# Kernel tuning notes

Measured on AMD Instinct MI355X. Metric: run time of the kernel, lower is better.

Reference implementation:

```python
import jax, jax.numpy as jnp
import numpy as np

N_NODES = 100000
N_EDGES = 600000
FEAT_DIM = 128


def setup_inputs() -> dict:
    key = jax.random.key(0)
    k_x, k_e, k_w1, k_b1, k_w2, k_b2 = jax.random.split(key, 6)
    x = jax.random.normal(k_x, (N_NODES, FEAT_DIM), dtype=jnp.float32)
    edge_index = jax.random.randint(k_e, (2, N_EDGES), 0, N_NODES, dtype=jnp.int64)
    # nn.Linear default init: U(-1/sqrt(fan_in), 1/sqrt(fan_in))
    lim1 = 1.0 / np.sqrt(2 * FEAT_DIM)
    lim2 = 1.0 / np.sqrt(FEAT_DIM)
    W1 = jax.random.uniform(k_w1, (2 * FEAT_DIM, FEAT_DIM), minval=-lim1, maxval=lim1, dtype=jnp.float32)
    b1 = jax.random.uniform(k_b1, (FEAT_DIM,), minval=-lim1, maxval=lim1, dtype=jnp.float32)
    W2 = jax.random.uniform(k_w2, (FEAT_DIM, 1), minval=-lim2, maxval=lim2, dtype=jnp.float32)
    b2 = jax.random.uniform(k_b2, (1,), minval=-lim2, maxval=lim2, dtype=jnp.float32)
    return {"x": x, "edge_index": edge_index, "W1": W1, "b1": b1, "W2": W2, "b2": b2}


def reference(x, edge_index, W1, b1, W2, b2):
    row, col = edge_index[0], edge_index[1]
    # gather endpoint features and concat -> [E, 2*feat_dim]
    edge_feat = jnp.concatenate([x[row], x[col]], axis=1)
    h = jax.nn.relu(edge_feat @ W1 + b1)  # [E, feat_dim]
    return jax.nn.sigmoid(h @ W2 + b2)    # [E, 1]
```

## Files before the change

kernel.cpp:

```cpp
#include <hip/hip_runtime.h>
#include <stdint.h>

#define N_NODES 100000
#define N_EDGES 600000
#define FEAT 128
#define BLK_M 128

typedef __attribute__((ext_vector_type(8))) short short8;
typedef __attribute__((ext_vector_type(4))) float floatx4;
typedef __attribute__((ext_vector_type(2))) float floatx2;

__device__ __forceinline__ short f2bf(float f) {
    unsigned u = __builtin_bit_cast(unsigned, f);
    u = (u + 0x7FFFu + ((u >> 16) & 1u)) >> 16;
    return (short)u;
}

__global__ __launch_bounds__(512, 4) void node_gemm_kernel(
    const float* __restrict__ x, const float* __restrict__ w1,
    const float* __restrict__ b1, unsigned char* __restrict__ y)
{
    __shared__ short lds_b[16 * 256 * 8];

    const int tid  = threadIdx.x;
    const int lane = tid & 63;
    const int wave = tid >> 6;
    const int nl   = lane & 15;
    const int q    = lane >> 4;
    const int m0   = blockIdx.x * BLK_M + wave * 16;

    const int node = m0 + nl;
    const int nsrc = (node < N_NODES) ? node : 0;
    floatx4 xv[8];
#pragma unroll
    for (int s = 0; s < 4; ++s) {
        const float* p = x + (size_t)nsrc * FEAT + s * 32 + q * 8;
        xv[2 * s]     = *(const floatx4*)(p);
        xv[2 * s + 1] = *(const floatx4*)(p + 4);
    }

#pragma unroll
    for (int it = 0; it < 8; ++it) {
        int t = it * 512 + tid;
        int n = t & 255, c = t >> 8;
        const float* src = (n < 128) ? (w1 + (c * 8) * 128 + n)
                                     : (w1 + (128 + c * 8) * 128 + (n - 128));
        short8 v;
#pragma unroll
        for (int j = 0; j < 8; ++j) v[j] = f2bf(src[j * 128]);
        *(short8*)(lds_b + t * 8) = v;
    }

    __syncthreads();

    short8 a[4];
#pragma unroll
    for (int s = 0; s < 4; ++s) {
        short8 av;
#pragma unroll
        for (int j = 0; j < 8; ++j) av[j] = f2bf(xv[2 * s + (j >> 2)][j & 3]);
        a[s] = av;
    }

    floatx4 acc[16];
#pragma unroll
    for (int nt = 0; nt < 16; ++nt) acc[nt] = (floatx4)(0.0f);

#pragma unroll
    for (int s = 0; s < 4; ++s) {
        const int crow = (s * 4 + q) << 8;
#pragma unroll
        for (int nt = 0; nt < 16; ++nt) {
            short8 wf = *(const short8*)(lds_b + ((crow + nt * 16 + nl) << 3));
            acc[nt] = __builtin_amdgcn_mfma_f32_16x16x32_bf16(wf, a[s], acc[nt], 0, 0, 0);
        }
    }

    if (node < N_NODES) {
        unsigned char* yr = y + (size_t)node * 256 + q * 4;
#pragma unroll
        for (int nt = 0; nt < 8; ++nt) {
            floatx4 bb = *(const floatx4*)(b1 + nt * 16 + q * 4);
            int d = __builtin_amdgcn_cvt_pk_fp8_f32(acc[nt][0] + bb[0],
                                                    acc[nt][1] + bb[1], 0, false);
            d = __builtin_amdgcn_cvt_pk_fp8_f32(acc[nt][2] + bb[2],
                                                acc[nt][3] + bb[3], d, true);
            *(int*)(yr + nt * 16) = d;
        }
#pragma unroll
        for (int nt = 8; nt < 16; ++nt) {
            int d = __builtin_amdgcn_cvt_pk_fp8_f32(acc[nt][0], acc[nt][1], 0, false);
            d = __builtin_amdgcn_cvt_pk_fp8_f32(acc[nt][2], acc[nt][3], d, true);
            *(int*)(yr + nt * 16) = d;
        }
    }
}

__device__ __forceinline__ void dec8(uint2 w, float* f) {
    floatx2 p0 = __builtin_amdgcn_cvt_pk_f32_fp8(w.x, false);
    floatx2 p1 = __builtin_amdgcn_cvt_pk_f32_fp8(w.x, true);
    floatx2 p2 = __builtin_amdgcn_cvt_pk_f32_fp8(w.y, false);
    floatx2 p3 = __builtin_amdgcn_cvt_pk_f32_fp8(w.y, true);
    f[0] = p0.x; f[1] = p0.y; f[2] = p1.x; f[3] = p1.y;
    f[4] = p2.x; f[5] = p2.y; f[6] = p3.x; f[7] = p3.y;
}

__global__ __launch_bounds__(256) void edge_kernel(
    const unsigned char* __restrict__ y, const int* __restrict__ eidx,
    const float* __restrict__ w2, const float* __restrict__ b2,
    float* __restrict__ out)
{
    const int l = threadIdx.x & 15;

    float w2r[8];
#pragma unroll
    for (int j = 0; j < 8; ++j) w2r[j] = w2[l * 8 + j];
    const float bias2 = b2[0];

    const int slot   = blockIdx.x * 16 + (threadIdx.x >> 4);
    const int nslots = gridDim.x * 16;

    for (int eb = slot * 4; eb < N_EDGES; eb += nslots * 4) {
        int4 rr = *(const int4*)(eidx + eb);
        int4 cc = *(const int4*)(eidx + N_EDGES + eb);

        uint2 u0 = *(const uint2*)(y + (size_t)rr.x * 256 + l * 8);
        uint2 u1 = *(const uint2*)(y + (size_t)rr.y * 256 + l * 8);
        uint2 u2 = *(const uint2*)(y + (size_t)rr.z * 256 + l * 8);
        uint2 u3 = *(const uint2*)(y + (size_t)rr.w * 256 + l * 8);
        uint2 v0 = *(const uint2*)(y + (size_t)cc.x * 256 + 128 + l * 8);
        uint2 v1 = *(const uint2*)(y + (size_t)cc.y * 256 + 128 + l * 8);
        uint2 v2 = *(const uint2*)(y + (size_t)cc.z * 256 + 128 + l * 8);
        uint2 v3 = *(const uint2*)(y + (size_t)cc.w * 256 + 128 + l * 8);

        float fu[8], fv[8];
        float p0 = 0.0f, p1 = 0.0f, p2 = 0.0f, p3 = 0.0f;

        dec8(u0, fu); dec8(v0, fv);
#pragma unroll
        for (int j = 0; j < 8; ++j)
            p0 = fmaf(fmaxf(fu[j] + fv[j], 0.0f), w2r[j], p0);
        dec8(u1, fu); dec8(v1, fv);
#pragma unroll
        for (int j = 0; j < 8; ++j)
            p1 = fmaf(fmaxf(fu[j] + fv[j], 0.0f), w2r[j], p1);
        dec8(u2, fu); dec8(v2, fv);
#pragma unroll
        for (int j = 0; j < 8; ++j)
            p2 = fmaf(fmaxf(fu[j] + fv[j], 0.0f), w2r[j], p2);
        dec8(u3, fu); dec8(v3, fv);
#pragma unroll
        for (int j = 0; j < 8; ++j)
            p3 = fmaf(fmaxf(fu[j] + fv[j], 0.0f), w2r[j], p3);

#pragma unroll
        for (int d = 1; d < 16; d <<= 1) {
            p0 += __shfl_xor(p0, d);
            p1 += __shfl_xor(p1, d);
            p2 += __shfl_xor(p2, d);
            p3 += __shfl_xor(p3, d);
        }

        if (l == 0) {
            floatx4 o;
            o[0] = 1.0f / (1.0f + __expf(-(p0 + bias2)));
            o[1] = 1.0f / (1.0f + __expf(-(p1 + bias2)));
            o[2] = 1.0f / (1.0f + __expf(-(p2 + bias2)));
            o[3] = 1.0f / (1.0f + __expf(-(p3 + bias2)));
            *(floatx4*)(out + eb) = o;
        }
    }
}

extern "C" void kernel_launch(void* const* d_in, const int* in_sizes, int n_in,
                              void* d_out, int out_size, void* d_ws, size_t ws_size,
                              hipStream_t stream) {
    const float* x  = (const float*)d_in[0];
    const int*   ei = (const int*)d_in[1];
    const float* W1 = (const float*)d_in[2];
    const float* b1 = (const float*)d_in[3];
    const float* W2 = (const float*)d_in[4];
    const float* b2 = (const float*)d_in[5];
    float* out = (float*)d_out;

    unsigned char* yq = (unsigned char*)d_ws;

    int mblocks = (N_NODES + BLK_M - 1) / BLK_M;
    node_gemm_kernel<<<mblocks, 512, 0, stream>>>(x, W1, b1, yq);

    edge_kernel<<<2048, 256, 0, stream>>>(yq, ei, W2, b2, out);
}
```

Before: 137.7 us.

## Make node GEMM persistent with register prefetch of next tile's x rows

```diff
diff --git a/kernel.cpp b/kernel.cpp
--- a/kernel.cpp
+++ b/kernel.cpp
@@ -5,6 +5,8 @@
 #define N_EDGES 600000
 #define FEAT 128
 #define BLK_M 128
+#define NT 782
+#define GRID_G 256
 
 typedef __attribute__((ext_vector_type(8))) short short8;
 typedef __attribute__((ext_vector_type(4))) float floatx4;
@@ -16,7 +18,7 @@
     return (short)u;
 }
 
-__global__ __launch_bounds__(512, 4) void node_gemm_kernel(
+__global__ __launch_bounds__(512, 2) void node_gemm_kernel(
     const float* __restrict__ x, const float* __restrict__ w1,
     const float* __restrict__ b1, unsigned char* __restrict__ y)
 {
@@ -27,17 +29,6 @@
     const int wave = tid >> 6;
     const int nl   = lane & 15;
     const int q    = lane >> 4;
-    const int m0   = blockIdx.x * BLK_M + wave * 16;
-
-    const int node = m0 + nl;
-    const int nsrc = (node < N_NODES) ? node : 0;
-    floatx4 xv[8];
-#pragma unroll
-    for (int s = 0; s < 4; ++s) {
-        const float* p = x + (size_t)nsrc * FEAT + s * 32 + q * 8;
-        xv[2 * s]     = *(const floatx4*)(p);
-        xv[2 * s + 1] = *(const floatx4*)(p + 4);
-    }
 
 #pragma unroll
     for (int it = 0; it < 8; ++it) {
@@ -51,47 +42,82 @@
         *(short8*)(lds_b + t * 8) = v;
     }
 
+    float b1v[8][4];
+#pragma unroll
+    for (int nt = 0; nt < 8; ++nt) {
+        floatx4 bb = *(const floatx4*)(b1 + nt * 16 + q * 4);
+        b1v[nt][0] = bb[0]; b1v[nt][1] = bb[1]; b1v[nt][2] = bb[2]; b1v[nt][3] = bb[3];
+    }
+
+    int task = blockIdx.x;
+    floatx4 xv[8];
+    {
+        int node = task * BLK_M + wave * 16 + nl;
+        int nsrc = (node < N_NODES) ? node : 0;
+        const float* p = x + (size_t)nsrc * FEAT + q * 8;
+#pragma unroll
+        for (int s = 0; s < 4; ++s) {
+            xv[2 * s]     = *(const floatx4*)(p + s * 32);
+            xv[2 * s + 1] = *(const floatx4*)(p + s * 32 + 4);
+        }
+    }
+
     __syncthreads();
 
-    short8 a[4];
-#pragma unroll
-    for (int s = 0; s < 4; ++s) {
-        short8 av;
-#pragma unroll
-        for (int j = 0; j < 8; ++j) av[j] = f2bf(xv[2 * s + (j >> 2)][j & 3]);
-        a[s] = av;
-    }
-
-    floatx4 acc[16];
-#pragma unroll
-    for (int nt = 0; nt < 16; ++nt) acc[nt] = (floatx4)(0.0f);
-
-#pragma unroll
-    for (int s = 0; s < 4; ++s) {
-        const int crow = (s * 4 + q) << 8;
-#pragma unroll
-        for (int nt = 0; nt < 16; ++nt) {
-            short8 wf = *(const short8*)(lds_b + ((crow + nt * 16 + nl) << 3));
-            acc[nt] = __builtin_amdgcn_mfma_f32_16x16x32_bf16(wf, a[s], acc[nt], 0, 0, 0);
-        }
-    }
-
-    if (node < N_NODES) {
-        unsigned char* yr = y + (size_t)node * 256 + q * 4;
-#pragma unroll
-        for (int nt = 0; nt < 8; ++nt) {
-            floatx4 bb = *(const floatx4*)(b1 + nt * 16 + q * 4);
-            int d = __builtin_amdgcn_cvt_pk_fp8_f32(acc[nt][0] + bb[0],
-                                                    acc[nt][1] + bb[1], 0, false);
-            d = __builtin_amdgcn_cvt_pk_fp8_f32(acc[nt][2] + bb[2],
-                                                acc[nt][3] + bb[3], d, true);
-            *(int*)(yr + nt * 16) = d;
-        }
-#pragma unroll
-        for (int nt = 8; nt < 16; ++nt) {
-            int d = __builtin_amdgcn_cvt_pk_fp8_f32(acc[nt][0], acc[nt][1], 0, false);
-            d = __builtin_amdgcn_cvt_pk_fp8_f32(acc[nt][2], acc[nt][3], d, true);
-            *(int*)(yr + nt * 16) = d;
+    for (; task < NT; task += GRID_G) {
+        const int node = task * BLK_M + wave * 16 + nl;
+
+        short8 a[4];
+#pragma unroll
+        for (int s = 0; s < 4; ++s) {
+            short8 av;
+#pragma unroll
+            for (int j = 0; j < 8; ++j) av[j] = f2bf(xv[2 * s + (j >> 2)][j & 3]);
+            a[s] = av;
+        }
+
+        const int task2 = task + GRID_G;
+        if (task2 < NT) {
+            int node2 = task2 * BLK_M + wave * 16 + nl;
+            int nsrc = (node2 < N_NODES) ? node2 : 0;
+            const float* p = x + (size_t)nsrc * FEAT + q * 8;
+#pragma unroll
+            for (int s = 0; s < 4; ++s) {
+                xv[2 * s]     = *(const floatx4*)(p + s * 32);
+                xv[2 * s + 1] = *(const floatx4*)(p + s * 32 + 4);
+            }
+        }
+
+        floatx4 acc[16];
+#pragma unroll
+        for (int nt = 0; nt < 16; ++nt) acc[nt] = (floatx4)(0.0f);
+
+#pragma unroll
+        for (int s = 0; s < 4; ++s) {
+            const int crow = (s * 4 + q) << 8;
+#pragma unroll
+            for (int nt = 0; nt < 16; ++nt) {
+                short8 wf = *(const short8*)(lds_b + ((crow + nt * 16 + nl) << 3));
+                acc[nt] = __builtin_amdgcn_mfma_f32_16x16x32_bf16(wf, a[s], acc[nt], 0, 0, 0);
+            }
+        }
+
+        if (node < N_NODES) {
+            unsigned char* yr = y + (size_t)node * 256 + q * 4;
+#pragma unroll
+            for (int nt = 0; nt < 8; ++nt) {
+                int d = __builtin_amdgcn_cvt_pk_fp8_f32(acc[nt][0] + b1v[nt][0],
+                                                        acc[nt][1] + b1v[nt][1], 0, false);
+                d = __builtin_amdgcn_cvt_pk_fp8_f32(acc[nt][2] + b1v[nt][2],
+                                                    acc[nt][3] + b1v[nt][3], d, true);
+                *(int*)(yr + nt * 16) = d;
+            }
+#pragma unroll
+            for (int nt = 8; nt < 16; ++nt) {
+                int d = __builtin_amdgcn_cvt_pk_fp8_f32(acc[nt][0], acc[nt][1], 0, false);
+                d = __builtin_amdgcn_cvt_pk_fp8_f32(acc[nt][2], acc[nt][3], d, true);
+                *(int*)(yr + nt * 16) = d;
+            }
         }
     }
 }
@@ -185,8 +211,6 @@
 
     unsigned char* yq = (unsigned char*)d_ws;
 
-    int mblocks = (N_NODES + BLK_M - 1) / BLK_M;
-    node_gemm_kernel<<<mblocks, 512, 0, stream>>>(x, W1, b1, yq);
-
+    node_gemm_kernel<<<GRID_G, 512, 0, stream>>>(x, W1, b1, yq);
     edge_kernel<<<2048, 256, 0, stream>>>(yq, ei, W2, b2, out);
 }
```

Result: slower. 207.9 us (+51.0%).
